# Kernel tuning notes

Measured on AMD Instinct MI355X. Metric: run time of the kernel, lower is better.

The kernel has to match this reference:

```python
import jax, jax.numpy as jnp
import numpy as np

N, E, B = 20000, 320000, 128
IN_DIM, HID, HEADS = 64, 64, 4
D = HID * HEADS          # 256 = conv output width (concat heads)
CAT = HID + 2 * D        # 576 = dueling head input
ENC_H, DUEL_H = 512, 128
NEG_SLOPE = 0.2


def setup_inputs() -> dict:
    key = jax.random.key(0)
    ks = jax.random.split(key, 30)
    g = lambda i, shape: jax.random.normal(ks[i], shape, dtype=jnp.float32) * 0.05
    return {
        "x": jax.random.normal(ks[0], (N, IN_DIM), dtype=jnp.float32),
        "edge_index": jax.random.randint(ks[1], (2, E), 0, N, dtype=jnp.int32),
        "indices": jax.random.randint(ks[2], (B,), 0, N, dtype=jnp.int32),
        # encoder MLP: input_dim -> 512 -> hidden_dim
        "enc_w1": g(3, (IN_DIM, ENC_H)), "enc_b1": g(4, (ENC_H,)),
        "enc_w2": g(5, (ENC_H, HID)),   "enc_b2": g(6, (HID,)),
        # GATv2 conv1: HID -> HID per head, HEADS heads
        "wl1": g(7, (HID, D)),  "bl1": g(8, (D,)),
        "wr1": g(9, (HID, D)),  "br1": g(10, (D,)),
        "att1": g(11, (HEADS, HID)), "bias1": g(12, (D,)),
        # GATv2 conv2: D -> HID per head, HEADS heads
        "wl2": g(13, (D, D)),   "bl2": g(14, (D,)),
        "wr2": g(15, (D, D)),   "br2": g(16, (D,)),
        "att2": g(17, (HEADS, HID)), "bias2": g(18, (D,)),
        # dueling heads: CAT -> 128 -> {2, 1}
        "q_w1": g(19, (CAT, DUEL_H)), "q_b1": g(20, (DUEL_H,)),
        "q_w2": g(21, (DUEL_H, 2)),   "q_b2": g(22, (2,)),
        "v_w1": g(23, (CAT, DUEL_H)), "v_b1": g(24, (DUEL_H,)),
        "v_w2": g(25, (DUEL_H, 1)),   "v_b2": g(26, (1,)),
    }


def _gatv2(h, src, dst, wl, bl, wr, br, att, bias):
    # PyG GATv2Conv: e_ij = att . leaky_relu(Wl h_j + Wr h_i); softmax over
    # incoming edges of each target i; out_i = sum_j alpha_ij * (Wl h_j).
    xl = (h @ wl + bl).reshape(-1, HEADS, HID)  # source transform
    xr = (h @ wr + br).reshape(-1, HEADS, HID)  # target transform
    e = jax.nn.leaky_relu(xl[src] + xr[dst], NEG_SLOPE)      # [E', H, D]
    score = jnp.einsum('ehd,hd->eh', e, att)                 # [E', H]
    m = jax.ops.segment_max(score, dst, num_segments=N)      # stable softmax
    ex = jnp.exp(score - m[dst])
    denom = jax.ops.segment_sum(ex, dst, num_segments=N)
    alpha = ex / (denom[dst] + 1e-16)                        # [E', H]
    out = jax.ops.segment_sum(alpha[:, :, None] * xl[src], dst, num_segments=N)
    return out.reshape(-1, D) + bias


def _forward(x, edge_index, indices,
             enc_w1, enc_b1, enc_w2, enc_b2,
             wl1, bl1, wr1, br1, att1, bias1,
             wl2, bl2, wr2, br2, att2, bias2,
             q_w1, q_b1, q_w2, q_b2, v_w1, v_b1, v_w2, v_b2):
    loops = jnp.arange(N, dtype=edge_index.dtype)  # add_self_loops=True
    src = jnp.concatenate([edge_index[0], loops])
    dst = jnp.concatenate([edge_index[1], loops])

    h = jax.nn.relu(x @ enc_w1 + enc_b1)
    h = jax.nn.relu(h @ enc_w2 + enc_b2)          # encoder + F.relu
    x1 = h[indices]
    h = jax.nn.relu(_gatv2(h, src, dst, wl1, bl1, wr1, br1, att1, bias1))
    x2 = h[indices]
    h = jax.nn.relu(_gatv2(h, src, dst, wl2, bl2, wr2, br2, att2, bias2))
    x3 = h[indices]

    feat = jnp.concatenate([x1, x2, x3], axis=1)  # [B, CAT]
    q = jax.nn.relu(feat @ q_w1 + q_b1) @ q_w2 + q_b2  # [B, 2]
    v = jax.nn.relu(feat @ v_w1 + v_b1) @ v_w2 + v_b2  # [B, 1]
    return q - q.mean(axis=1, keepdims=True) + v


def reference(x, edge_index, indices,
              enc_w1, enc_b1, enc_w2, enc_b2,
              wl1, bl1, wr1, br1, att1, bias1,
              wl2, bl2, wr2, br2, att2, bias2,
              q_w1, q_b1, q_w2, q_b2, v_w1, v_b1, v_w2, v_b2):
    return _forward(x, edge_index, indices,
                    enc_w1, enc_b1, enc_w2, enc_b2,
                    wl1, bl1, wr1, br1, att1, bias1,
                    wl2, bl2, wr2, br2, att2, bias2,
                    q_w1, q_b1, q_w2, q_b2, v_w1, v_b1, v_w2, v_b2)
```

## Files before the change

### kernel.cpp

```cpp
#include <hip/hip_runtime.h>

#define IN_DIM 64
#define HID 64
#define HEADS 4
#define DD 256
#define ENC_H 512
#define DUEL_H 128
#define NEG_SLOPE 0.2f

typedef _Float16 f16;
typedef __attribute__((ext_vector_type(2))) _Float16 f16x2;
typedef __attribute__((ext_vector_type(4))) _Float16 f16x4;
typedef __attribute__((ext_vector_type(8))) _Float16 f16x8;
typedef __attribute__((ext_vector_type(4))) float f32x4;

__device__ __forceinline__ f16x2 u2h(unsigned u) {
    union { unsigned u; f16x2 h; } c; c.u = u; return c.h;
}
__device__ __forceinline__ unsigned h2u(f16x2 h) {
    union { unsigned u; f16x2 h; } c; c.h = h; return c.u;
}


__global__ void prep_all(
    const float4* __restrict__ x, f16x4* __restrict__ x16, int nx4,
    const float* __restrict__ w1, const float* __restrict__ w2,
    const float* __restrict__ wl1, const float* __restrict__ wr1,
    const float* __restrict__ wl2, const float* __restrict__ wr2,
    f16* __restrict__ w1t, f16* __restrict__ w2t,
    f16* __restrict__ wcat1, f16* __restrict__ wcat2,
    f16* __restrict__ wr2nt,
    int* __restrict__ counts, int ncnt) {
    int i = blockIdx.x * blockDim.x + threadIdx.x;
    if (i < nx4) {
        float4 v = x[i];
        f16x4 o = {(f16)v.x, (f16)v.y, (f16)v.z, (f16)v.w};
        x16[i] = o;
        return;
    }
    i -= nx4;
    if (i < 229376) {
        if (i < 32768) {
            int k = i >> 9, n = i & 511;
            w1t[n * 64 + k] = (f16)w1[i];
        } else if (i < 65536) {
            int j = i - 32768; int k = j >> 6, n = j & 63;
            w2t[n * 512 + k] = (f16)w2[j];
        } else if (i < 81920) {
            int j = i - 65536; int k = j >> 8, n = j & 255;
            wcat1[n * 64 + k] = (f16)wl1[j];
        } else if (i < 98304) {
            int j = i - 81920; int k = j >> 8, n = j & 255;
            wcat1[(256 + n) * 64 + k] = (f16)wr1[j];
        } else if (i < 163840) {
            int j = i - 98304; int k = j >> 8, n = j & 255;
            wcat2[n * 256 + k] = (f16)wl2[j];
        } else {
            int j = i - 163840;
            wr2nt[j] = (f16)wr2[j];
        }
        return;
    }
    i -= 229376;
    if (i < ncnt) counts[i] = 0;
}


template <int K, int BN>
struct GemmCfg {
    static constexpr int SB = K + 8;
    static constexpr int CE = BN / 2 + 8;
    static constexpr int SLABSZ = BN * SB;
    static constexpr int EPISZ = 4 * 32 * CE;
    static constexpr int SMEMSZ = SLABSZ > EPISZ ? SLABSZ : EPISZ;
};

template <int K, int BN>
__device__ __forceinline__ void gemm_body(
    int bx, int by, f16* __restrict__ smem,
    const f16* __restrict__ A, const f16* __restrict__ Bt,
    const float* __restrict__ biasA, const float* __restrict__ biasB, int NS,
    int M, int relu,
    f16* __restrict__ C1, f16* __restrict__ C2) {
    constexpr int KS = K / 32;
    constexpr int PF = (KS < 8) ? KS : 8;
    constexpr int COLW = BN / 2;
    constexpr int NT = COLW / 16;
    constexpr int SB = GemmCfg<K, BN>::SB;
    constexpr int CE = GemmCfg<K, BN>::CE;

    f16* Bs = smem;
    int tid = threadIdx.x;
    int wave = tid >> 6, lane = tid & 63;
    int quad = lane >> 4, l16 = lane & 15;
    int wr = wave >> 1, wc = wave & 1;
    int row0 = by * 64;
    int col0 = bx * BN;

    constexpr int NCH = BN * K / 8;
#pragma unroll
    for (int i = 0; i < NCH / 256; ++i) {
        int c = tid + i * 256;
        int r = c / (K / 8), ko = (c % (K / 8)) * 8;
        uint4 v = *(const uint4*)&Bt[(size_t)(col0 + r) * K + ko];
        *(uint4*)&Bs[r * SB + ko] = v;
    }
    __syncthreads();

    const f16* Aptr[2];
#pragma unroll
    for (int mt = 0; mt < 2; ++mt) {
        int arow = row0 + wr * 32 + mt * 16 + l16;
        if (arow >= M) arow = M - 1;
        Aptr[mt] = &A[(size_t)arow * K + quad * 8];
    }

    f32x4 acc[2][NT];
#pragma unroll
    for (int mt = 0; mt < 2; ++mt)
#pragma unroll
        for (int j = 0; j < NT; ++j) acc[mt][j] = (f32x4){0.f, 0.f, 0.f, 0.f};

    f16x8 afb[2][PF];
#pragma unroll
    for (int mt = 0; mt < 2; ++mt)
#pragma unroll
        for (int i = 0; i < PF; ++i)
            afb[mt][i] = *(const f16x8*)&Aptr[mt][i * 32];

#pragma unroll
    for (int s = 0; s < KS; ++s) {
        f16x8 af0 = afb[0][s % PF], af1 = afb[1][s % PF];
        if (s + PF < KS) {
            afb[0][s % PF] = *(const f16x8*)&Aptr[0][(s + PF) * 32];
            afb[1][s % PF] = *(const f16x8*)&Aptr[1][(s + PF) * 32];
        }
        const f16* bbase = &Bs[(size_t)(wc * COLW) * SB + s * 32 + quad * 8];
#pragma unroll
        for (int nt = 0; nt < NT; ++nt) {
            f16x8 bf = *(const f16x8*)&bbase[(nt * 16 + l16) * SB];
            acc[0][nt] = __builtin_amdgcn_mfma_f32_16x16x32_f16(af0, bf, acc[0][nt], 0, 0, 0);
            acc[1][nt] = __builtin_amdgcn_mfma_f32_16x16x32_f16(af1, bf, acc[1][nt], 0, 0, 0);
        }
    }

    __syncthreads();
    f16* ep = &smem[wave * 32 * CE];
#pragma unroll
    for (int mt = 0; mt < 2; ++mt)
#pragma unroll
        for (int nt = 0; nt < NT; ++nt) {
            int gcol = col0 + wc * COLW + nt * 16 + l16;
            float bb = (gcol < NS) ? biasA[gcol] : biasB[gcol - NS];
#pragma unroll
            for (int r = 0; r < 4; ++r) {
                float v = acc[mt][nt][r] + bb;
                if (relu) v = fmaxf(v, 0.f);
                ep[(mt * 16 + quad * 4 + r) * CE + nt * 16 + l16] = (f16)v;
            }
        }
    constexpr int CPR = COLW / 8;
    constexpr int NPASS = (32 * CPR) / 64;
#pragma unroll
    for (int i = 0; i < NPASS; ++i) {
        int u = lane + i * 64;
        int row = u / CPR, seg = u % CPR;
        uint4 v = *(const uint4*)&ep[row * CE + seg * 8];
        int grow = row0 + wr * 32 + row;
        int gcol = col0 + wc * COLW + seg * 8;
        if (grow < M) {
            if (gcol < NS) *(uint4*)&C1[(size_t)grow * NS + gcol] = v;
            else           *(uint4*)&C2[(size_t)grow * NS + (gcol - NS)] = v;
        }
    }
}

template <int K, int BN>
__global__ __launch_bounds__(256) void gemm_slab(
    const f16* __restrict__ A, const f16* __restrict__ Bt,
    const float* __restrict__ biasA, const float* __restrict__ biasB, int NS,
    int M, int relu,
    f16* __restrict__ C1, f16* __restrict__ C2) {
    __shared__ __align__(16) f16 smem[GemmCfg<K, BN>::SMEMSZ];
    gemm_body<K, BN>(blockIdx.x, blockIdx.y, smem, A, Bt, biasA, biasB, NS, M, relu, C1, C2);
}


__device__ __forceinline__ void hist_body(int auxbid, const int* __restrict__ ei,
                                          int E, int N, int* __restrict__ counts) {
    int e = auxbid * 256 + threadIdx.x;
    int Etot = E + N;
    if (e >= Etot) return;
    int dst = (e < E) ? ei[E + e] : (e - E);
    atomicAdd(&counts[dst], 1);
}

__device__ __forceinline__ void scatter_body(int auxbid, const int* __restrict__ ei,
                                             int E, int N, int* __restrict__ cursor,
                                             int* __restrict__ csr_src) {
    int e = auxbid * 256 + threadIdx.x;
    int Etot = E + N;
    if (e >= Etot) return;
    int src, dst;
    if (e < E) { src = ei[e]; dst = ei[E + e]; }
    else       { src = e - E; dst = e - E; }
    int pos = atomicAdd(&cursor[dst], 1);
    csr_src[pos] = src;
}

__device__ void scan_body(int* __restrict__ tile, const int* __restrict__ counts,
                          int* __restrict__ offsets, int* __restrict__ cursor, int n) {
    __shared__ int wsum[4];
    const int t = threadIdx.x;
    const int lane = t & 63, wid = t >> 6;
    int running = 0;
    for (int base = 0; base < n; base += 2048) {
        const int cnt = (n - base < 2048) ? (n - base) : 2048;
        int nv4 = cnt >> 2;
        for (int i = t; i < nv4; i += 256)
            ((int4*)tile)[i] = ((const int4*)(counts + base))[i];
        for (int i = (nv4 << 2) + t; i < cnt; i += 256)
            tile[i] = counts[base + i];
        __syncthreads();

        int e0 = t * 8;
        int nj = cnt - e0; if (nj < 0) nj = 0; if (nj > 8) nj = 8;
        int v8[8];
        int s = 0;
#pragma unroll
        for (int j = 0; j < 8; ++j) {
            int val = (j < nj) ? tile[e0 + j] : 0;
            v8[j] = val; s += val;
        }
        int v = s;
        for (int off = 1; off < 64; off <<= 1) {
            int u = __shfl_up(v, off);
            if (lane >= off) v += u;
        }
        if (lane == 63) wsum[wid] = v;
        __syncthreads();
        int wadd = 0, tot = 0;
#pragma unroll
        for (int w = 0; w < 4; ++w) {
            int ws = wsum[w];
            if (w < wid) wadd += ws;
            tot += ws;
        }
        int excl = v - s + wadd;
        int run = running + excl;
        int o8[8];
#pragma unroll
        for (int j = 0; j < 8; ++j) { o8[j] = run; run += v8[j]; }
        if (nj == 8) {
            int4 a = make_int4(o8[0], o8[1], o8[2], o8[3]);
            int4 b = make_int4(o8[4], o8[5], o8[6], o8[7]);
            *(int4*)&offsets[base + e0]     = a;
            *(int4*)&offsets[base + e0 + 4] = b;
            *(int4*)&cursor[base + e0]      = a;
            *(int4*)&cursor[base + e0 + 4]  = b;
        } else {
            for (int j = 0; j < nj; ++j) {
                offsets[base + e0 + j] = o8[j];
                cursor[base + e0 + j]  = o8[j];
            }
        }
        running += tot;
        __syncthreads();
    }
    if (t == 0) offsets[n] = running;
}

__global__ __launch_bounds__(256) void enc1_hist_kernel(
    const f16* __restrict__ A, const f16* __restrict__ Bt,
    const float* __restrict__ bias, int M, f16* __restrict__ C, int gemmBlocks,
    const int* __restrict__ ei, int E, int N, int* __restrict__ counts) {
    __shared__ __align__(16) f16 smem[GemmCfg<64, 128>::SMEMSZ];
    int bid = blockIdx.x;
    if (bid < gemmBlocks)
        gemm_body<64, 128>(bid & 3, bid >> 2, smem, A, Bt, bias, bias, 512, M, 1, C, C);
    else
        hist_body(bid - gemmBlocks, ei, E, N, counts);
}

__global__ __launch_bounds__(256) void enc2_scan_kernel(
    const f16* __restrict__ A, const f16* __restrict__ Bt,
    const float* __restrict__ bias, int M, f16* __restrict__ C, int gemmBlocks,
    const int* __restrict__ counts, int* __restrict__ offsets,
    int* __restrict__ cursor, int n) {
    constexpr int GB = GemmCfg<512, 64>::SMEMSZ * 2;
    constexpr int SB = 2048 * 4;
    constexpr int PB = GB > SB ? GB : SB;
    __shared__ __align__(16) char pool[PB];
    int bid = blockIdx.x;
    if (bid < gemmBlocks)
        gemm_body<512, 64>(0, bid, (f16*)pool, A, Bt, bias, bias, 64, M, 1, C, C);
    else
        scan_body((int*)pool, counts, offsets, cursor, n);
}

__global__ __launch_bounds__(256) void conv1t_scatter_kernel(
    const f16* __restrict__ A, const f16* __restrict__ Bt,
    const float* __restrict__ biasA, const float* __restrict__ biasB, int M,
    f16* __restrict__ C1, f16* __restrict__ C2, int gemmBlocks,
    const int* __restrict__ ei, int E, int N,
    int* __restrict__ cursor, int* __restrict__ csr_src) {
    __shared__ __align__(16) f16 smem[GemmCfg<64, 128>::SMEMSZ];
    int bid = blockIdx.x;
    if (bid < gemmBlocks)
        gemm_body<64, 128>(bid & 3, bid >> 2, smem, A, Bt, biasA, biasB, DD, M, 0, C1, C2);
    else
        scatter_body(bid - gemmBlocks, ei, E, N, cursor, csr_src);
}


__global__ __launch_bounds__(256) void gat_fused_kernel(
    const uint4* __restrict__ xl, const uint4* __restrict__ xr,
    const float4* __restrict__ att,
    const int* __restrict__ offsets, const int* __restrict__ csr_src,
    const float4* __restrict__ bias, uint4* __restrict__ h16, int N) {
    int node = (blockIdx.x * blockDim.x + threadIdx.x) >> 6;
    int lane = threadIdx.x & 63;
    int half = lane >> 5, l32 = lane & 31;
    if (node >= N) return;
    int s = offsets[node], e = offsets[node + 1];
    uint4 xrw = xr[(size_t)node * 32 + l32];
    f16x2 xr0 = u2h(xrw.x), xr1 = u2h(xrw.y), xr2 = u2h(xrw.z), xr3 = u2h(xrw.w);
    float4 awA = att[l32 * 2], awB = att[l32 * 2 + 1];
    f16x2 a6[4] = {{(f16)(0.6f * awA.x), (f16)(0.6f * awA.y)},
                   {(f16)(0.6f * awA.z), (f16)(0.6f * awA.w)},
                   {(f16)(0.6f * awB.x), (f16)(0.6f * awB.y)},
                   {(f16)(0.6f * awB.z), (f16)(0.6f * awB.w)}};
    f16x2 a4[4] = {{(f16)(0.4f * awA.x), (f16)(0.4f * awA.y)},
                   {(f16)(0.4f * awA.z), (f16)(0.4f * awA.w)},
                   {(f16)(0.4f * awB.x), (f16)(0.4f * awB.y)},
                   {(f16)(0.4f * awB.z), (f16)(0.4f * awB.w)}};
    float denom = 0.f;
    float acc0 = 0.f, acc1 = 0.f, acc2 = 0.f, acc3 = 0.f;
    float acc4 = 0.f, acc5 = 0.f, acc6 = 0.f, acc7 = 0.f;

    auto edge_dot = [&](uint4 raw) -> float {
        f16x2 t0 = u2h(raw.x) + xr0, t1 = u2h(raw.y) + xr1;
        f16x2 t2 = u2h(raw.z) + xr2, t3 = u2h(raw.w) + xr3;
        float d = __builtin_amdgcn_fdot2(t0, a6[0], 0.f, false);
        d = __builtin_amdgcn_fdot2(u2h(h2u(t0) & 0x7FFF7FFFu), a4[0], d, false);
        d = __builtin_amdgcn_fdot2(t1, a6[1], d, false);
        d = __builtin_amdgcn_fdot2(u2h(h2u(t1) & 0x7FFF7FFFu), a4[1], d, false);
        d = __builtin_amdgcn_fdot2(t2, a6[2], d, false);
        d = __builtin_amdgcn_fdot2(u2h(h2u(t2) & 0x7FFF7FFFu), a4[2], d, false);
        d = __builtin_amdgcn_fdot2(t3, a6[3], d, false);
        d = __builtin_amdgcn_fdot2(u2h(h2u(t3) & 0x7FFF7FFFu), a4[3], d, false);
        return d;
    };
    auto accum = [&](uint4 raw, float ee) {
        f16x2 v0 = u2h(raw.x), v1 = u2h(raw.y), v2 = u2h(raw.z), v3 = u2h(raw.w);
        acc0 = fmaf(ee, (float)v0.x, acc0); acc1 = fmaf(ee, (float)v0.y, acc1);
        acc2 = fmaf(ee, (float)v1.x, acc2); acc3 = fmaf(ee, (float)v1.y, acc3);
        acc4 = fmaf(ee, (float)v2.x, acc4); acc5 = fmaf(ee, (float)v2.y, acc5);
        acc6 = fmaf(ee, (float)v3.x, acc6); acc7 = fmaf(ee, (float)v3.y, acc7);
    };

    int p = s + half;
    for (; p + 6 < e; p += 8) {
        uint4 raw[4];
#pragma unroll
        for (int j = 0; j < 4; ++j)
            raw[j] = xl[(size_t)csr_src[p + j * 2] * 32 + l32];
        float sc[4];
#pragma unroll
        for (int j = 0; j < 4; ++j) sc[j] = edge_dot(raw[j]);
#pragma unroll
        for (int j = 0; j < 4; ++j) sc[j] += __shfl_xor(sc[j], 1);
#pragma unroll
        for (int j = 0; j < 4; ++j) sc[j] += __shfl_xor(sc[j], 2);
#pragma unroll
        for (int j = 0; j < 4; ++j) sc[j] += __shfl_xor(sc[j], 4);
#pragma unroll
        for (int j = 0; j < 4; ++j) {
            float ee = __expf(sc[j]);
            denom += ee;
            accum(raw[j], ee);
        }
    }
    for (; p < e; p += 2) {
        uint4 raw = xl[(size_t)csr_src[p] * 32 + l32];
        float d = edge_dot(raw);
        d += __shfl_xor(d, 1);
        d += __shfl_xor(d, 2);
        d += __shfl_xor(d, 4);
        float ee = __expf(d);
        denom += ee;
        accum(raw, ee);
    }
    denom += __shfl_xor(denom, 32);
    acc0 += __shfl_xor(acc0, 32); acc1 += __shfl_xor(acc1, 32);
    acc2 += __shfl_xor(acc2, 32); acc3 += __shfl_xor(acc3, 32);
    acc4 += __shfl_xor(acc4, 32); acc5 += __shfl_xor(acc5, 32);
    acc6 += __shfl_xor(acc6, 32); acc7 += __shfl_xor(acc7, 32);

    if (half == 0) {
        float inv = 1.f / (denom + 1e-16f);
        float4 bbA = bias[l32 * 2], bbB = bias[l32 * 2 + 1];
        float o0 = fmaxf(fmaf(acc0, inv, bbA.x), 0.f);
        float o1 = fmaxf(fmaf(acc1, inv, bbA.y), 0.f);
        float o2 = fmaxf(fmaf(acc2, inv, bbA.z), 0.f);
        float o3 = fmaxf(fmaf(acc3, inv, bbA.w), 0.f);
        float o4 = fmaxf(fmaf(acc4, inv, bbB.x), 0.f);
        float o5 = fmaxf(fmaf(acc5, inv, bbB.y), 0.f);
        float o6 = fmaxf(fmaf(acc6, inv, bbB.z), 0.f);
        float o7 = fmaxf(fmaf(acc7, inv, bbB.w), 0.f);
        f16x2 h0 = {(f16)o0, (f16)o1}, h1 = {(f16)o2, (f16)o3};
        f16x2 h2 = {(f16)o4, (f16)o5}, h3 = {(f16)o6, (f16)o7};
        uint4 outw = make_uint4(h2u(h0), h2u(h1), h2u(h2), h2u(h3));
        h16[(size_t)node * 32 + l32] = outw;
    }
}


__global__ __launch_bounds__(1024) void gat2_head_kernel(
    const uint4* __restrict__ xl, const f16* __restrict__ hC1,
    const f16* __restrict__ wr2nt, const float* __restrict__ br2,
    const float4* __restrict__ att,
    const int* __restrict__ indices,
    const int* __restrict__ offsets, const int* __restrict__ csr_src,
    const float* __restrict__ bias2, const f16* __restrict__ hE16,
    const float* __restrict__ qw1, const float* __restrict__ qb1,
    const float* __restrict__ qw2, const float* __restrict__ qb2,
    const float* __restrict__ vw1, const float* __restrict__ vb1,
    const float* __restrict__ vw2, const float* __restrict__ vb2,
    float* __restrict__ out) {
    __shared__ float feat[576];
    __shared__ float xrs[256];
    __shared__ float partial[4][256];
    __shared__ float pden[16][32];
    __shared__ float pacc[16][32][8];
    __shared__ float red[384];
    int b = blockIdx.x;
    int t = threadIdx.x;
    int wave = t >> 6, lane = t & 63;
    int half = lane >> 5, l32 = lane & 31;
    int node = indices[b];

    if (t < 320) {
        feat[t] = (t < 64) ? (float)hE16[(size_t)node * 64 + t]
                           : (float)hC1[(size_t)node * 256 + t - 64];
    }
    __syncthreads();

    {
        int o = t & 255, kq = t >> 8;
        const f16* w = &wr2nt[(size_t)(kq * 64) * 256 + o];
        const float* f = &feat[64 + kq * 64];
        float a0 = 0.f, a1 = 0.f;
#pragma unroll
        for (int k = 0; k < 64; k += 2) {
            a0 = fmaf(f[k],     (float)w[(size_t)k * 256],       a0);
            a1 = fmaf(f[k + 1], (float)w[(size_t)(k + 1) * 256], a1);
        }
        partial[kq][o] = a0 + a1;
    }
    __syncthreads();
    if (t < 256)
        xrs[t] = partial[0][t] + partial[1][t] + partial[2][t] + partial[3][t] + br2[t];
    __syncthreads();

    f16x2 xr0 = {(f16)xrs[l32 * 8 + 0], (f16)xrs[l32 * 8 + 1]};
    f16x2 xr1 = {(f16)xrs[l32 * 8 + 2], (f16)xrs[l32 * 8 + 3]};
    f16x2 xr2 = {(f16)xrs[l32 * 8 + 4], (f16)xrs[l32 * 8 + 5]};
    f16x2 xr3 = {(f16)xrs[l32 * 8 + 6], (f16)xrs[l32 * 8 + 7]};

    int s = offsets[node], e = offsets[node + 1];
    float4 awA = att[l32 * 2], awB = att[l32 * 2 + 1];
    f16x2 a6[4] = {{(f16)(0.6f * awA.x), (f16)(0.6f * awA.y)},
                   {(f16)(0.6f * awA.z), (f16)(0.6f * awA.w)},
                   {(f16)(0.6f * awB.x), (f16)(0.6f * awB.y)},
                   {(f16)(0.6f * awB.z), (f16)(0.6f * awB.w)}};
    f16x2 a4[4] = {{(f16)(0.4f * awA.x), (f16)(0.4f * awA.y)},
                   {(f16)(0.4f * awA.z), (f16)(0.4f * awA.w)},
                   {(f16)(0.4f * awB.x), (f16)(0.4f * awB.y)},
                   {(f16)(0.4f * awB.z), (f16)(0.4f * awB.w)}};
    float denom = 0.f;
    float acc0 = 0.f, acc1 = 0.f, acc2 = 0.f, acc3 = 0.f;
    float acc4 = 0.f, acc5 = 0.f, acc6 = 0.f, acc7 = 0.f;

    auto edge_dot = [&](uint4 raw) -> float {
        f16x2 t0 = u2h(raw.x) + xr0, t1 = u2h(raw.y) + xr1;
        f16x2 t2 = u2h(raw.z) + xr2, t3 = u2h(raw.w) + xr3;
        float d = __builtin_amdgcn_fdot2(t0, a6[0], 0.f, false);
        d = __builtin_amdgcn_fdot2(u2h(h2u(t0) & 0x7FFF7FFFu), a4[0], d, false);
        d = __builtin_amdgcn_fdot2(t1, a6[1], d, false);
        d = __builtin_amdgcn_fdot2(u2h(h2u(t1) & 0x7FFF7FFFu), a4[1], d, false);
        d = __builtin_amdgcn_fdot2(t2, a6[2], d, false);
        d = __builtin_amdgcn_fdot2(u2h(h2u(t2) & 0x7FFF7FFFu), a4[2], d, false);
        d = __builtin_amdgcn_fdot2(t3, a6[3], d, false);
        d = __builtin_amdgcn_fdot2(u2h(h2u(t3) & 0x7FFF7FFFu), a4[3], d, false);
        return d;
    };
    auto accum = [&](uint4 raw, float ee) {
        f16x2 v0 = u2h(raw.x), v1 = u2h(raw.y), v2 = u2h(raw.z), v3 = u2h(raw.w);
        acc0 = fmaf(ee, (float)v0.x, acc0); acc1 = fmaf(ee, (float)v0.y, acc1);
        acc2 = fmaf(ee, (float)v1.x, acc2); acc3 = fmaf(ee, (float)v1.y, acc3);
        acc4 = fmaf(ee, (float)v2.x, acc4); acc5 = fmaf(ee, (float)v2.y, acc5);
        acc6 = fmaf(ee, (float)v3.x, acc6); acc7 = fmaf(ee, (float)v3.y, acc7);
    };

    for (int p = s + (wave << 1) + half; p < e; p += 32) {
        uint4 raw = xl[(size_t)csr_src[p] * 32 + l32];
        float d = edge_dot(raw);
        d += __shfl_xor(d, 1);
        d += __shfl_xor(d, 2);
        d += __shfl_xor(d, 4);
        float ee = __expf(d);
        denom += ee;
        accum(raw, ee);
    }
    denom += __shfl_xor(denom, 32);
    acc0 += __shfl_xor(acc0, 32); acc1 += __shfl_xor(acc1, 32);
    acc2 += __shfl_xor(acc2, 32); acc3 += __shfl_xor(acc3, 32);
    acc4 += __shfl_xor(acc4, 32); acc5 += __shfl_xor(acc5, 32);
    acc6 += __shfl_xor(acc6, 32); acc7 += __shfl_xor(acc7, 32);
    if (half == 0) {
        pden[wave][l32] = denom;
        pacc[wave][l32][0] = acc0; pacc[wave][l32][1] = acc1;
        pacc[wave][l32][2] = acc2; pacc[wave][l32][3] = acc3;
        pacc[wave][l32][4] = acc4; pacc[wave][l32][5] = acc5;
        pacc[wave][l32][6] = acc6; pacc[wave][l32][7] = acc7;
    }
    __syncthreads();

    if (t < 256) {
        int lw = t >> 3, d = t & 7;
        float den = 0.f, a = 0.f;
#pragma unroll
        for (int w = 0; w < 16; ++w) { den += pden[w][lw]; a += pacc[w][lw][d]; }
        float inv = 1.f / (den + 1e-16f);
        feat[320 + t] = fmaxf(fmaf(a, inv, bias2[t]), 0.f);
    }
    __syncthreads();

    {
        int o = t & 255, kq = t >> 8;
        int k0 = kq * 144;
        float a0 = 0.f, a1 = 0.f;
        if (o < 128) {
            const float* w = &qw1[(size_t)k0 * 128 + o];
            const float* f = &feat[k0];
#pragma unroll
            for (int k = 0; k < 144; k += 2) {
                a0 = fmaf(f[k],     w[(size_t)k * 128],       a0);
                a1 = fmaf(f[k + 1], w[(size_t)(k + 1) * 128], a1);
            }
        } else {
            const float* w = &vw1[(size_t)k0 * 128 + (o - 128)];
            const float* f = &feat[k0];
#pragma unroll
            for (int k = 0; k < 144; k += 2) {
                a0 = fmaf(f[k],     w[(size_t)k * 128],       a0);
                a1 = fmaf(f[k + 1], w[(size_t)(k + 1) * 128], a1);
            }
        }
        partial[kq][o] = a0 + a1;
    }
    __syncthreads();
    if (t < 256) {
        float s4 = partial[0][t] + partial[1][t] + partial[2][t] + partial[3][t];
        if (t < 128) {
            float aq = fmaxf(s4 + qb1[t], 0.f);
            red[t]       = aq * qw2[t * 2 + 0];
            red[128 + t] = aq * qw2[t * 2 + 1];
        } else {
            int tv = t - 128;
            float av = fmaxf(s4 + vb1[tv], 0.f);
            red[256 + tv] = av * vw2[tv];
        }
    }
    __syncthreads();
    for (int s2 = 64; s2 > 0; s2 >>= 1) {
        if (t < s2) {
            red[t] += red[t + s2];
            red[128 + t] += red[128 + t + s2];
            red[256 + t] += red[256 + t + s2];
        }
        __syncthreads();
    }
    if (t == 0) {
        float q0 = red[0] + qb2[0];
        float q1 = red[128] + qb2[1];
        float v  = red[256] + vb2[0];
        float mean = 0.5f * (q0 + q1);
        out[b * 2 + 0] = q0 - mean + v;
        out[b * 2 + 1] = q1 - mean + v;
    }
}


extern "C" void kernel_launch(void* const* d_in, const int* in_sizes, int n_in,
                              void* d_out, int out_size, void* d_ws, size_t ws_size,
                              hipStream_t stream) {
    const float* x      = (const float*)d_in[0];
    const int*   ei     = (const int*)d_in[1];
    const int*   indices= (const int*)d_in[2];
    const float* enc_w1 = (const float*)d_in[3];
    const float* enc_b1 = (const float*)d_in[4];
    const float* enc_w2 = (const float*)d_in[5];
    const float* enc_b2 = (const float*)d_in[6];
    const float* wl1    = (const float*)d_in[7];
    const float* bl1    = (const float*)d_in[8];
    const float* wr1    = (const float*)d_in[9];
    const float* br1    = (const float*)d_in[10];
    const float* att1   = (const float*)d_in[11];
    const float* bias1  = (const float*)d_in[12];
    const float* wl2    = (const float*)d_in[13];
    const float* bl2    = (const float*)d_in[14];
    const float* wr2    = (const float*)d_in[15];
    const float* br2    = (const float*)d_in[16];
    const float* att2   = (const float*)d_in[17];
    const float* bias2  = (const float*)d_in[18];
    const float* qw1    = (const float*)d_in[19];
    const float* qb1    = (const float*)d_in[20];
    const float* qw2    = (const float*)d_in[21];
    const float* qb2    = (const float*)d_in[22];
    const float* vw1    = (const float*)d_in[23];
    const float* vb1    = (const float*)d_in[24];
    const float* vw2    = (const float*)d_in[25];
    const float* vb2    = (const float*)d_in[26];

    const int N = in_sizes[0] / IN_DIM;
    const int E = in_sizes[1] / 2;
    const int B = in_sizes[2];
    const int Etot = E + N;

    char* wsb = (char*)d_ws;
    size_t off = 0;
    auto alloc = [&](size_t bytes) -> void* {
        void* p = wsb + off;
        off = (off + bytes + 255) & ~(size_t)255;
        return p;
    };
    f16* x16     = (f16*)alloc((size_t)N * 64 * 2);
    f16* h1_16   = (f16*)alloc((size_t)N * 512 * 2);
    f16* hE16    = (f16*)alloc((size_t)N * 64 * 2);
    f16* xl16    = (f16*)alloc((size_t)N * 256 * 2);
    f16* xr16    = (f16*)alloc((size_t)N * 256 * 2);
    f16* hC1_16  = (f16*)alloc((size_t)N * 256 * 2);
    f16* w1t     = (f16*)alloc((size_t)ENC_H * IN_DIM * 2);
    f16* w2t     = (f16*)alloc((size_t)HID * ENC_H * 2);
    f16* wcat1   = (f16*)alloc((size_t)512 * HID * 2);
    f16* wcat2   = (f16*)alloc((size_t)512 * DD * 2);
    f16* wr2nt   = (f16*)alloc((size_t)DD * DD * 2);
    int* counts  = (int*)alloc((size_t)(N + 1) * 4);
    int* offsets = (int*)alloc((size_t)(N + 1) * 4);
    int* cursor  = (int*)alloc((size_t)(N + 1) * 4);
    int* csr_src = (int*)alloc((size_t)Etot * 4);

    int nx4 = N * 16;
    int ntot = nx4 + 229376 + (N + 1);
    prep_all<<<(ntot + 255) / 256, 256, 0, stream>>>(
        (const float4*)x, (f16x4*)x16, nx4,
        enc_w1, enc_w2, wl1, wr1, wl2, wr2,
        w1t, w2t, wcat1, wcat2, wr2nt, counts, N + 1);

    int grows = (N + 63) / 64;
    int gemmB1 = 4 * grows;
    int auxB = (Etot + 255) / 256;

    enc1_hist_kernel<<<gemmB1 + auxB, 256, 0, stream>>>(
        x16, w1t, enc_b1, N, h1_16, gemmB1, ei, E, N, counts);

    enc2_scan_kernel<<<grows + 1, 256, 0, stream>>>(
        h1_16, w2t, enc_b2, N, hE16, grows, counts, offsets, cursor, N);

    conv1t_scatter_kernel<<<gemmB1 + auxB, 256, 0, stream>>>(
        hE16, wcat1, bl1, br1, N, xl16, xr16, gemmB1, ei, E, N, cursor, csr_src);

    int gatg = (N * 64 + 255) / 256;
    gat_fused_kernel<<<gatg, 256, 0, stream>>>(
        (const uint4*)xl16, (const uint4*)xr16, (const float4*)att1,
        offsets, csr_src, (const float4*)bias1, (uint4*)hC1_16, N);

    gemm_slab<256, 128><<<dim3(2, grows), dim3(256), 0, stream>>>(
        hC1_16, wcat2, bl2, bl2, DD, N, 0, xl16, xl16);

    gat2_head_kernel<<<B, 1024, 0, stream>>>(
        (const uint4*)xl16, hC1_16, wr2nt, br2, (const float4*)att2,
        indices, offsets, csr_src, bias2, hE16,
        qw1, qb1, qw2, qb2, vw1, vb1, vw2, vb2, (float*)d_out);
}
```

Before: 224.3 us.

## Restrict conv1 aggregation and conv2 transform to needed 1-hop source set

```diff
diff --git a/kernel.cpp b/kernel.cpp
--- a/kernel.cpp
+++ b/kernel.cpp
@@ -30,7 +30,7 @@
     f16* __restrict__ w1t, f16* __restrict__ w2t,
     f16* __restrict__ wcat1, f16* __restrict__ wcat2,
     f16* __restrict__ wr2nt,
-    int* __restrict__ counts, int ncnt) {
+    int* __restrict__ zeros, int nz) {
     int i = blockIdx.x * blockDim.x + threadIdx.x;
     if (i < nx4) {
         float4 v = x[i];
@@ -62,7 +62,7 @@
         return;
     }
     i -= 229376;
-    if (i < ncnt) counts[i] = 0;
+    if (i < nz) zeros[i] = 0;
 }
 
 
@@ -175,14 +175,98 @@
     }
 }
 
-template <int K, int BN>
-__global__ __launch_bounds__(256) void gemm_slab(
+
+__global__ __launch_bounds__(256) void conv2t_gather_kernel(
     const f16* __restrict__ A, const f16* __restrict__ Bt,
-    const float* __restrict__ biasA, const float* __restrict__ biasB, int NS,
-    int M, int relu,
-    f16* __restrict__ C1, f16* __restrict__ C2) {
+    const float* __restrict__ bias,
+    const int* __restrict__ wlist, const int* __restrict__ wcnt,
+    f16* __restrict__ C) {
+    constexpr int K = 256, BN = 128;
+    constexpr int KS = K / 32, PF = 8;
+    constexpr int COLW = BN / 2, NT = COLW / 16;
+    constexpr int SB = GemmCfg<K, BN>::SB;
+    constexpr int CE = GemmCfg<K, BN>::CE;
     __shared__ __align__(16) f16 smem[GemmCfg<K, BN>::SMEMSZ];
-    gemm_body<K, BN>(blockIdx.x, blockIdx.y, smem, A, Bt, biasA, biasB, NS, M, relu, C1, C2);
+
+    int M_c = wcnt[0];
+    int row0 = blockIdx.y * 64;
+    if (row0 >= M_c) return;
+
+    f16* Bs = smem;
+    int tid = threadIdx.x;
+    int wave = tid >> 6, lane = tid & 63;
+    int quad = lane >> 4, l16 = lane & 15;
+    int wr = wave >> 1, wc = wave & 1;
+    int col0 = blockIdx.x * BN;
+
+    constexpr int NCH = BN * K / 8;
+#pragma unroll
+    for (int i = 0; i < NCH / 256; ++i) {
+        int c = tid + i * 256;
+        int r = c / (K / 8), ko = (c % (K / 8)) * 8;
+        uint4 v = *(const uint4*)&Bt[(size_t)(col0 + r) * K + ko];
+        *(uint4*)&Bs[r * SB + ko] = v;
+    }
+    __syncthreads();
+
+    const f16* Aptr[2];
+#pragma unroll
+    for (int mt = 0; mt < 2; ++mt) {
+        int crow = row0 + wr * 32 + mt * 16 + l16;
+        if (crow >= M_c) crow = M_c - 1;
+        int arow = wlist[crow];
+        Aptr[mt] = &A[(size_t)arow * K + quad * 8];
+    }
+
+    f32x4 acc[2][NT];
+#pragma unroll
+    for (int mt = 0; mt < 2; ++mt)
+#pragma unroll
+        for (int j = 0; j < NT; ++j) acc[mt][j] = (f32x4){0.f, 0.f, 0.f, 0.f};
+
+    f16x8 afb[2][PF];
+#pragma unroll
+    for (int mt = 0; mt < 2; ++mt)
+#pragma unroll
+        for (int i = 0; i < PF; ++i)
+            afb[mt][i] = *(const f16x8*)&Aptr[mt][i * 32];
+
+#pragma unroll
+    for (int s = 0; s < KS; ++s) {
+        f16x8 af0 = afb[0][s % PF], af1 = afb[1][s % PF];
+        const f16* bbase = &Bs[(size_t)(wc * COLW) * SB + s * 32 + quad * 8];
+#pragma unroll
+        for (int nt = 0; nt < NT; ++nt) {
+            f16x8 bf = *(const f16x8*)&bbase[(nt * 16 + l16) * SB];
+            acc[0][nt] = __builtin_amdgcn_mfma_f32_16x16x32_f16(af0, bf, acc[0][nt], 0, 0, 0);
+            acc[1][nt] = __builtin_amdgcn_mfma_f32_16x16x32_f16(af1, bf, acc[1][nt], 0, 0, 0);
+        }
+    }
+
+    __syncthreads();
+    f16* ep = &smem[wave * 32 * CE];
+#pragma unroll
+    for (int mt = 0; mt < 2; ++mt)
+#pragma unroll
+        for (int nt = 0; nt < NT; ++nt) {
+            int gcol = col0 + wc * COLW + nt * 16 + l16;
+            float bb = bias[gcol];
+#pragma unroll
+            for (int r = 0; r < 4; ++r)
+                ep[(mt * 16 + quad * 4 + r) * CE + nt * 16 + l16] =
+                    (f16)(acc[mt][nt][r] + bb);
+        }
+    constexpr int CPR = COLW / 8;
+    constexpr int NPASS = (32 * CPR) / 64;
+#pragma unroll
+    for (int i = 0; i < NPASS; ++i) {
+        int u = lane + i * 64;
+        int row = u / CPR, seg = u % CPR;
+        uint4 v = *(const uint4*)&ep[row * CE + seg * 8];
+        int grow = row0 + wr * 32 + row;
+        int gcol = col0 + wc * COLW + seg * 8;
+        if (grow < M_c) *(uint4*)&C[(size_t)grow * DD + gcol] = v;
+    }
 }
 
 
@@ -206,6 +290,17 @@
     else       { src = e - E; dst = e - E; }
     int pos = atomicAdd(&cursor[dst], 1);
     csr_src[pos] = src;
+}
+
+__device__ __forceinline__ void wappend(int src, int* __restrict__ inW,
+                                        int* __restrict__ wcnt,
+                                        int* __restrict__ wlist,
+                                        int* __restrict__ mapv) {
+    if (atomicExch(&inW[src], 1) == 0) {
+        int c = atomicAdd(wcnt, 1);
+        wlist[c] = src;
+        mapv[src] = c;
+    }
 }
 
 __device__ void scan_body(int* __restrict__ tile, const int* __restrict__ counts,
@@ -273,9 +368,21 @@
 __global__ __launch_bounds__(256) void enc1_hist_kernel(
     const f16* __restrict__ A, const f16* __restrict__ Bt,
     const float* __restrict__ bias, int M, f16* __restrict__ C, int gemmBlocks,
-    const int* __restrict__ ei, int E, int N, int* __restrict__ counts) {
+    const int* __restrict__ ei, int E, int N, int* __restrict__ counts,
+    const int* __restrict__ indices, int B,
+    int* __restrict__ s0f, int* __restrict__ inW, int* __restrict__ wcnt,
+    int* __restrict__ wlist, int* __restrict__ mapv) {
     __shared__ __align__(16) f16 smem[GemmCfg<64, 128>::SMEMSZ];
     int bid = blockIdx.x;
+    if (bid == (int)gridDim.x - 1) {
+        int t = threadIdx.x;
+        if (t < B) {
+            int src = indices[t];
+            s0f[src] = 1;
+            wappend(src, inW, wcnt, wlist, mapv);
+        }
+        return;
+    }
     if (bid < gemmBlocks)
         gemm_body<64, 128>(bid & 3, bid >> 2, smem, A, Bt, bias, bias, 512, M, 1, C, C);
     else
@@ -286,16 +393,26 @@
     const f16* __restrict__ A, const f16* __restrict__ Bt,
     const float* __restrict__ bias, int M, f16* __restrict__ C, int gemmBlocks,
     const int* __restrict__ counts, int* __restrict__ offsets,
-    int* __restrict__ cursor, int n) {
+    int* __restrict__ cursor, int n,
+    const int* __restrict__ ei, int E,
+    const int* __restrict__ s0f, int* __restrict__ inW, int* __restrict__ wcnt,
+    int* __restrict__ wlist, int* __restrict__ mapv) {
     constexpr int GB = GemmCfg<512, 64>::SMEMSZ * 2;
     constexpr int SB = 2048 * 4;
     constexpr int PB = GB > SB ? GB : SB;
     __shared__ __align__(16) char pool[PB];
     int bid = blockIdx.x;
-    if (bid < gemmBlocks)
+    if (bid < gemmBlocks) {
         gemm_body<512, 64>(0, bid, (f16*)pool, A, Bt, bias, bias, 64, M, 1, C, C);
-    else
+    } else if (bid == gemmBlocks) {
         scan_body((int*)pool, counts, offsets, cursor, n);
+    } else {
+        int e = (bid - gemmBlocks - 1) * 256 + threadIdx.x;
+        if (e < E) {
+            int dst = ei[E + e];
+            if (s0f[dst]) wappend(ei[e], inW, wcnt, wlist, mapv);
+        }
+    }
 }
 
 __global__ __launch_bounds__(256) void conv1t_scatter_kernel(
@@ -317,11 +434,13 @@
     const uint4* __restrict__ xl, const uint4* __restrict__ xr,
     const float4* __restrict__ att,
     const int* __restrict__ offsets, const int* __restrict__ csr_src,
-    const float4* __restrict__ bias, uint4* __restrict__ h16, int N) {
+    const float4* __restrict__ bias, uint4* __restrict__ h16, int N,
+    const int* __restrict__ inW) {
     int node = (blockIdx.x * blockDim.x + threadIdx.x) >> 6;
     int lane = threadIdx.x & 63;
     int half = lane >> 5, l32 = lane & 31;
     if (node >= N) return;
+    if (!inW[node]) return;
     int s = offsets[node], e = offsets[node + 1];
     uint4 xrw = xr[(size_t)node * 32 + l32];
     f16x2 xr0 = u2h(xrw.x), xr1 = u2h(xrw.y), xr2 = u2h(xrw.z), xr3 = u2h(xrw.w);
@@ -420,7 +539,7 @@
     const uint4* __restrict__ xl, const f16* __restrict__ hC1,
     const f16* __restrict__ wr2nt, const float* __restrict__ br2,
     const float4* __restrict__ att,
-    const int* __restrict__ indices,
+    const int* __restrict__ indices, const int* __restrict__ mapv,
     const int* __restrict__ offsets, const int* __restrict__ csr_src,
     const float* __restrict__ bias2, const f16* __restrict__ hE16,
     const float* __restrict__ qw1, const float* __restrict__ qb1,
@@ -504,7 +623,8 @@
     };
 
     for (int p = s + (wave << 1) + half; p < e; p += 32) {
-        uint4 raw = xl[(size_t)csr_src[p] * 32 + l32];
+        int cidx = mapv[csr_src[p]];
+        uint4 raw = xl[(size_t)cidx * 32 + l32];
         float d = edge_dot(raw);
         d += __shfl_xor(d, 1);
         d += __shfl_xor(d, 2);
@@ -647,27 +767,37 @@
     f16* wcat1   = (f16*)alloc((size_t)512 * HID * 2);
     f16* wcat2   = (f16*)alloc((size_t)512 * DD * 2);
     f16* wr2nt   = (f16*)alloc((size_t)DD * DD * 2);
-    int* counts  = (int*)alloc((size_t)(N + 1) * 4);
+    int* zeros   = (int*)alloc((size_t)(3 * N + 17) * 4);
+    int* counts  = zeros;
+    int* s0f     = zeros + (N + 1);
+    int* inW     = s0f + N;
+    int* wcnt    = inW + N;
     int* offsets = (int*)alloc((size_t)(N + 1) * 4);
     int* cursor  = (int*)alloc((size_t)(N + 1) * 4);
     int* csr_src = (int*)alloc((size_t)Etot * 4);
+    int* wlist   = (int*)alloc((size_t)N * 4);
+    int* mapv    = (int*)alloc((size_t)N * 4);
 
     int nx4 = N * 16;
-    int ntot = nx4 + 229376 + (N + 1);
+    int nz = 3 * N + 17;
+    int ntot = nx4 + 229376 + nz;
     prep_all<<<(ntot + 255) / 256, 256, 0, stream>>>(
         (const float4*)x, (f16x4*)x16, nx4,
         enc_w1, enc_w2, wl1, wr1, wl2, wr2,
-        w1t, w2t, wcat1, wcat2, wr2nt, counts, N + 1);
+        w1t, w2t, wcat1, wcat2, wr2nt, zeros, nz);
 
     int grows = (N + 63) / 64;
     int gemmB1 = 4 * grows;
     int auxB = (Etot + 255) / 256;
-
-    enc1_hist_kernel<<<gemmB1 + auxB, 256, 0, stream>>>(
-        x16, w1t, enc_b1, N, h1_16, gemmB1, ei, E, N, counts);
-
-    enc2_scan_kernel<<<grows + 1, 256, 0, stream>>>(
-        h1_16, w2t, enc_b2, N, hE16, grows, counts, offsets, cursor, N);
+    int wscanB = (E + 255) / 256;
+
+    enc1_hist_kernel<<<gemmB1 + auxB + 1, 256, 0, stream>>>(
+        x16, w1t, enc_b1, N, h1_16, gemmB1, ei, E, N, counts,
+        indices, B, s0f, inW, wcnt, wlist, mapv);
+
+    enc2_scan_kernel<<<grows + 1 + wscanB, 256, 0, stream>>>(
+        h1_16, w2t, enc_b2, N, hE16, grows, counts, offsets, cursor, N,
+        ei, E, s0f, inW, wcnt, wlist, mapv);
 
     conv1t_scatter_kernel<<<gemmB1 + auxB, 256, 0, stream>>>(
         hE16, wcat1, bl1, br1, N, xl16, xr16, gemmB1, ei, E, N, cursor, csr_src);
@@ -675,13 +805,13 @@
     int gatg = (N * 64 + 255) / 256;
     gat_fused_kernel<<<gatg, 256, 0, stream>>>(
         (const uint4*)xl16, (const uint4*)xr16, (const float4*)att1,
-        offsets, csr_src, (const float4*)bias1, (uint4*)hC1_16, N);
-
-    gemm_slab<256, 128><<<dim3(2, grows), dim3(256), 0, stream>>>(
-        hC1_16, wcat2, bl2, bl2, DD, N, 0, xl16, xl16);
+        offsets, csr_src, (const float4*)bias1, (uint4*)hC1_16, N, inW);
+
+    conv2t_gather_kernel<<<dim3(2, grows), dim3(256), 0, stream>>>(
+        hC1_16, wcat2, bl2, wlist, wcnt, xl16);
 
     gat2_head_kernel<<<B, 1024, 0, stream>>>(
         (const uint4*)xl16, hC1_16, wr2nt, br2, (const float4*)att2,
-        indices, offsets, csr_src, bias2, hE16,
+        indices, mapv, offsets, csr_src, bias2, hE16,
         qw1, qb1, qw2, qb2, vw1, vb1, vw2, vb2, (float*)d_out);
 }
```

After: 212.8 us. -5.1%, faster.
